# Performance work log

Measured on AMD Instinct MI355X. Metric: run time of the kernel, lower is better.

Reference implementation:

```python
import jax, jax.numpy as jnp
import numpy as np

B, T, D, H = 64, 512, 2048, 512

def setup_inputs() -> dict:
    key = jax.random.key(0)
    k1, k2, k3, k4, k5 = jax.random.split(key, 5)
    hidden_frames = jax.random.normal(k1, (B, T, D), dtype=jnp.float32)
    hidden_text = jax.random.normal(k2, (B, D), dtype=jnp.float32)
    Wa = jax.random.normal(k3, (D, H), dtype=jnp.float32) * 0.01
    Ua = jax.random.normal(k4, (D, H), dtype=jnp.float32) * 0.01
    Va = jax.random.normal(k5, (H,), dtype=jnp.float32) * 0.01
    ba = jnp.zeros((1, 1, H), dtype=jnp.float32)
    return {"hidden_frames": hidden_frames, "hidden_text": hidden_text,
            "Wa": Wa, "Ua": Ua, "Va": Va, "ba": ba}

def reference(hidden_frames, hidden_text, Wa, Ua, Va, ba):
    # Uh: [B, 1, H]
    Uh = jnp.matmul(hidden_text, Ua)[:, None, :]
    # Ws: [B, T, H]
    Ws = jnp.einsum('btd,dh->bth', hidden_frames, Wa)
    # additive attention scores: [B, T]
    scores = jnp.einsum('bth,h->bt', jnp.tanh(Ws + Uh + ba), Va)
    att = jax.nn.softmax(scores, axis=1)  # [B, T]
    # weighted sum over frames: [B, D]
    return jnp.einsum('bt,btd->bd', att, hidden_frames)
```

## Files before the change

### kernel.cpp

```cpp
#include <hip/hip_runtime.h>
#include <hip/hip_bf16.h>
#include <stdint.h>

#define B_ 64
#define T_ 512
#define D_ 2048
#define H_ 512

typedef __bf16 bf16x8 __attribute__((ext_vector_type(8)));
typedef float floatx4 __attribute__((ext_vector_type(4)));

__device__ __forceinline__ unsigned short f2bf(float f) {
  unsigned int u = __float_as_uint(f);
  return (unsigned short)((u + 0x7FFFu + ((u >> 16) & 1u)) >> 16);
}
__device__ __forceinline__ unsigned int pack2(float a, float b) {
  return (unsigned int)f2bf(a) | ((unsigned int)f2bf(b) << 16);
}

__global__ void k_transpose_wa(const float* __restrict__ Wa,
                               unsigned short* __restrict__ WaT) {
  __shared__ float t[32][33];
  int h0 = blockIdx.x * 32;
  int d0 = blockIdx.y * 32;
  int j  = threadIdx.x & 31;
  int i0 = threadIdx.x >> 5;
#pragma unroll
  for (int ii = 0; ii < 4; ii++) {
    int i = i0 + ii * 8;
    t[i][j] = Wa[(size_t)(d0 + i) * H_ + h0 + j];
  }
  __syncthreads();
#pragma unroll
  for (int jj = 0; jj < 4; jj++) {
    int r = i0 + jj * 8;
    WaT[(size_t)(h0 + r) * D_ + d0 + j] = f2bf(t[j][r]);
  }
}

__global__ void k_uh(const float* __restrict__ text, const float* __restrict__ Ua,
                     float* __restrict__ UhB) {
  __shared__ float tloc[8][128];
  const int h  = blockIdx.x * 256 + threadIdx.x;
  const int b0 = blockIdx.y * 8;
  const int d0 = blockIdx.z * 128;
  {
    int r = threadIdx.x >> 5;
    int c = threadIdx.x & 31;
#pragma unroll
    for (int j = 0; j < 4; j++)
      tloc[r][c + 32 * j] = text[(size_t)(b0 + r) * D_ + d0 + c + 32 * j];
  }
  __syncthreads();
  float acc[8] = {0.f, 0.f, 0.f, 0.f, 0.f, 0.f, 0.f, 0.f};
#pragma unroll 4
  for (int dd = 0; dd < 128; dd++) {
    float ua = Ua[(size_t)(d0 + dd) * H_ + h];
#pragma unroll
    for (int i = 0; i < 8; i++) acc[i] = fmaf(tloc[i][dd], ua, acc[i]);
  }
#pragma unroll
  for (int i = 0; i < 8; i++) atomicAdd(&UhB[(b0 + i) * H_ + h], acc[i]);
}

__launch_bounds__(256, 2)
__global__ void k_scores(const float* __restrict__ frames,
                         const unsigned short* __restrict__ WaT,
                         const float* __restrict__ UhB,
                         const float* __restrict__ Va,
                         const float* __restrict__ ba,
                         float* __restrict__ scores) {
  __shared__ __align__(16) unsigned short ldsA[128 * 72];
  __shared__ __align__(16) unsigned short ldsB[128 * 72];
  const int tid  = threadIdx.x;
  const int lane = tid & 63, wave = tid >> 6;
  const int wm = wave >> 1, wn = wave & 1;
  const int lr = lane & 15, q = lane >> 4;
  const int mBase = blockIdx.x * 128;
  const int hBase = blockIdx.y * 128;

  floatx4 acc[4][4];
#pragma unroll
  for (int mi = 0; mi < 4; mi++)
#pragma unroll
    for (int ni = 0; ni < 4; ni++) acc[mi][ni] = (floatx4){0.f, 0.f, 0.f, 0.f};

  for (int k0 = 0; k0 < D_; k0 += 64) {
#pragma unroll
    for (int i = 0; i < 4; i++) {
      int task = i * 256 + tid;
      int m = task >> 3, oct = task & 7;
      const float* src = frames + (size_t)(mBase + m) * D_ + k0 + oct * 8;
      float4 p0 = ((const float4*)src)[0];
      float4 p1 = ((const float4*)src)[1];
      uint4 w;
      w.x = pack2(p0.x, p0.y); w.y = pack2(p0.z, p0.w);
      w.z = pack2(p1.x, p1.y); w.w = pack2(p1.z, p1.w);
      *reinterpret_cast<uint4*>(&ldsA[m * 72 + oct * 8]) = w;
    }
#pragma unroll
    for (int i = 0; i < 4; i++) {
      int task = i * 256 + tid;
      int n = task >> 3, oct = task & 7;
      uint4 w = *reinterpret_cast<const uint4*>(
          WaT + (size_t)(hBase + n) * D_ + k0 + oct * 8);
      *reinterpret_cast<uint4*>(&ldsB[n * 72 + oct * 8]) = w;
    }
    __syncthreads();
#pragma unroll
    for (int kk = 0; kk < 2; kk++) {
      bf16x8 af[4], bfr[4];
#pragma unroll
      for (int mi = 0; mi < 4; mi++)
        af[mi] = *reinterpret_cast<const bf16x8*>(
            &ldsA[(wm * 64 + mi * 16 + lr) * 72 + kk * 32 + q * 8]);
#pragma unroll
      for (int ni = 0; ni < 4; ni++)
        bfr[ni] = *reinterpret_cast<const bf16x8*>(
            &ldsB[(wn * 64 + ni * 16 + lr) * 72 + kk * 32 + q * 8]);
#pragma unroll
      for (int mi = 0; mi < 4; mi++)
#pragma unroll
        for (int ni = 0; ni < 4; ni++)
          acc[mi][ni] = __builtin_amdgcn_mfma_f32_16x16x32_bf16(
              af[mi], bfr[ni], acc[mi][ni], 0, 0, 0);
    }
    __syncthreads();
  }

  const int b = mBase >> 9;
  float uhv[4], vav[4];
#pragma unroll
  for (int ni = 0; ni < 4; ni++) {
    int h = hBase + wn * 64 + ni * 16 + lr;
    uhv[ni] = UhB[b * H_ + h] + ba[h];
    vav[ni] = Va[h];
  }
  const int rowBase = mBase + wm * 64;
#pragma unroll
  for (int mi = 0; mi < 4; mi++) {
#pragma unroll
    for (int reg = 0; reg < 4; reg++) {
      float s = 0.f;
#pragma unroll
      for (int ni = 0; ni < 4; ni++) {
        float x = acc[mi][ni][reg] + uhv[ni];
        float e = __expf(2.f * x);
        s += (1.f - 2.f / (e + 1.f)) * vav[ni];
      }
      s += __shfl_xor(s, 1, 16);
      s += __shfl_xor(s, 2, 16);
      s += __shfl_xor(s, 4, 16);
      s += __shfl_xor(s, 8, 16);
      if (lr == 0)
        atomicAdd(&scores[rowBase + mi * 16 + q * 4 + reg], s);
    }
  }
}

__global__ void k_softmax(const float* __restrict__ scores, float* __restrict__ att) {
  __shared__ float red[4];
  int b = blockIdx.x, tid = threadIdx.x;
  int lane = tid & 63, wave = tid >> 6;
  float s0 = scores[b * T_ + tid];
  float s1 = scores[b * T_ + 256 + tid];
  float mx = fmaxf(s0, s1);
#pragma unroll
  for (int off = 32; off; off >>= 1) mx = fmaxf(mx, __shfl_xor(mx, off, 64));
  if (lane == 0) red[wave] = mx;
  __syncthreads();
  mx = fmaxf(fmaxf(red[0], red[1]), fmaxf(red[2], red[3]));
  __syncthreads();
  float e0 = __expf(s0 - mx), e1 = __expf(s1 - mx);
  float sm = e0 + e1;
#pragma unroll
  for (int off = 32; off; off >>= 1) sm += __shfl_xor(sm, off, 64);
  if (lane == 0) red[wave] = sm;
  __syncthreads();
  sm = red[0] + red[1] + red[2] + red[3];
  float inv = 1.f / sm;
  att[b * T_ + tid]       = e0 * inv;
  att[b * T_ + 256 + tid] = e1 * inv;
}

__global__ void k_wsum(const float* __restrict__ frames, const float* __restrict__ att,
                       float* __restrict__ out) {
  int b  = blockIdx.y;
  int d0 = blockIdx.x * 1024 + threadIdx.x * 4;
  int t0 = blockIdx.z * (T_ / 4);
  const float* fp = frames + (size_t)b * T_ * D_ + d0;
  const float* ap = att + b * T_;
  float4 acc = {0.f, 0.f, 0.f, 0.f};
  for (int t = t0; t < t0 + T_ / 4; t += 4) {
    float a0 = ap[t], a1 = ap[t + 1], a2 = ap[t + 2], a3 = ap[t + 3];
    float4 v0 = *(const float4*)(fp + (size_t)(t + 0) * D_);
    float4 v1 = *(const float4*)(fp + (size_t)(t + 1) * D_);
    float4 v2 = *(const float4*)(fp + (size_t)(t + 2) * D_);
    float4 v3 = *(const float4*)(fp + (size_t)(t + 3) * D_);
    acc.x += a0 * v0.x + a1 * v1.x + a2 * v2.x + a3 * v3.x;
    acc.y += a0 * v0.y + a1 * v1.y + a2 * v2.y + a3 * v3.y;
    acc.z += a0 * v0.z + a1 * v1.z + a2 * v2.z + a3 * v3.z;
    acc.w += a0 * v0.w + a1 * v1.w + a2 * v2.w + a3 * v3.w;
  }
  float* op = out + (size_t)b * D_ + d0;
  atomicAdd(op + 0, acc.x);
  atomicAdd(op + 1, acc.y);
  atomicAdd(op + 2, acc.z);
  atomicAdd(op + 3, acc.w);
}

extern "C" void kernel_launch(void* const* d_in, const int* in_sizes, int n_in,
                              void* d_out, int out_size, void* d_ws, size_t ws_size,
                              hipStream_t stream) {
  const float* frames = (const float*)d_in[0];
  const float* text   = (const float*)d_in[1];
  const float* Wa     = (const float*)d_in[2];
  const float* Ua     = (const float*)d_in[3];
  const float* Va     = (const float*)d_in[4];
  const float* ba     = (const float*)d_in[5];
  float* out = (float*)d_out;

  char* ws = (char*)d_ws;
  unsigned short* WaT = (unsigned short*)ws;
  float* UhB    = (float*)(ws + (size_t)(2u << 20));
  float* scores = (float*)(ws + (size_t)(2u << 20) + (128u << 10));
  float* att    = (float*)(ws + (size_t)(2u << 20) + (256u << 10));

  (void)hipMemsetAsync(UhB, 0, (size_t)(256u << 10), stream);
  (void)hipMemsetAsync(out, 0, (size_t)B_ * D_ * sizeof(float), stream);

  k_transpose_wa<<<dim3(H_ / 32, D_ / 32), 256, 0, stream>>>(Wa, WaT);
  k_uh<<<dim3(H_ / 256, B_ / 8, D_ / 128), 256, 0, stream>>>(text, Ua, UhB);
  k_scores<<<dim3((B_ * T_) / 128, H_ / 128), 256, 0, stream>>>(frames, WaT, UhB, Va, ba, scores);
  k_softmax<<<B_, 256, 0, stream>>>(scores, att);
  k_wsum<<<dim3(D_ / 1024, B_, 4), 256, 0, stream>>>(frames, att, out);
}
```

Before: 630.5 us.

## Precast frames to bf16 and load GEMM tiles with direct global-to-LDS loads

Adds a pass that casts the fp32 frames to bf16 in the workspace once, so the scores GEMM, which rereads frames for each of four H tiles, reads half the bytes and skips the per-tile conversion. Both A and B tiles are now loaded with global_load_lds 16-byte transfers straight into LDS, and the LDS row padding goes from 72 to 64 elements to match. This costs an extra 256MB write and reread of the cast buffer, and the unpadded LDS layout may cause bank conflicts on the fragment reads. The cast path only runs if the workspace is large enough, otherwise the old fp32 path is kept.

Measured after the change: 579.8 us. 1.09x faster.

```diff
diff --git a/kernel.cpp b/kernel.cpp
--- a/kernel.cpp
+++ b/kernel.cpp
@@ -16,6 +16,12 @@
 }
 __device__ __forceinline__ unsigned int pack2(float a, float b) {
   return (unsigned int)f2bf(a) | ((unsigned int)f2bf(b) << 16);
+}
+
+__device__ __forceinline__ void gload16(const void* g, void* l) {
+  __builtin_amdgcn_global_load_lds(
+      (const __attribute__((address_space(1))) void*)g,
+      (__attribute__((address_space(3))) void*)l, 16, 0, 0);
 }
 
 __global__ void k_transpose_wa(const float* __restrict__ Wa,
@@ -36,6 +42,16 @@
     int r = i0 + jj * 8;
     WaT[(size_t)(h0 + r) * D_ + d0 + j] = f2bf(t[j][r]);
   }
+}
+
+__global__ void k_cast(const float* __restrict__ in, unsigned short* __restrict__ out) {
+  size_t i = ((size_t)blockIdx.x * 256 + threadIdx.x) * 8;
+  float4 a = ((const float4*)(in + i))[0];
+  float4 b = ((const float4*)(in + i))[1];
+  uint4 w;
+  w.x = pack2(a.x, a.y); w.y = pack2(a.z, a.w);
+  w.z = pack2(b.x, b.y); w.w = pack2(b.z, b.w);
+  *(uint4*)(out + i) = w;
 }
 
 __global__ void k_uh(const float* __restrict__ text, const float* __restrict__ Ua,
@@ -63,15 +79,16 @@
   for (int i = 0; i < 8; i++) atomicAdd(&UhB[(b0 + i) * H_ + h], acc[i]);
 }
 
+template <bool PRECAST>
 __launch_bounds__(256, 2)
-__global__ void k_scores(const float* __restrict__ frames,
+__global__ void k_scores(const void* __restrict__ framesAny,
                          const unsigned short* __restrict__ WaT,
                          const float* __restrict__ UhB,
                          const float* __restrict__ Va,
                          const float* __restrict__ ba,
                          float* __restrict__ scores) {
-  __shared__ __align__(16) unsigned short ldsA[128 * 72];
-  __shared__ __align__(16) unsigned short ldsB[128 * 72];
+  __shared__ __align__(16) unsigned short ldsA[128 * 64];
+  __shared__ __align__(16) unsigned short ldsB[128 * 64];
   const int tid  = threadIdx.x;
   const int lane = tid & 63, wave = tid >> 6;
   const int wm = wave >> 1, wn = wave & 1;
@@ -79,6 +96,8 @@
   const int mBase = blockIdx.x * 128;
   const int hBase = blockIdx.y * 128;
 
+  const int sRow = lane >> 3, sOct = lane & 7;
+
   floatx4 acc[4][4];
 #pragma unroll
   for (int mi = 0; mi < 4; mi++)
@@ -86,25 +105,34 @@
     for (int ni = 0; ni < 4; ni++) acc[mi][ni] = (floatx4){0.f, 0.f, 0.f, 0.f};
 
   for (int k0 = 0; k0 < D_; k0 += 64) {
+    if (PRECAST) {
+      const unsigned short* fb = (const unsigned short*)framesAny;
+#pragma unroll
+      for (int i = 0; i < 4; i++) {
+        int r0 = wave * 32 + i * 8;
+        gload16(fb + (size_t)(mBase + r0 + sRow) * D_ + k0 + sOct * 8,
+                &ldsA[r0 * 64]);
+      }
+    } else {
+      const float* ff = (const float*)framesAny;
+#pragma unroll
+      for (int i = 0; i < 4; i++) {
+        int task = i * 256 + tid;
+        int m = task >> 3, oct = task & 7;
+        const float* src = ff + (size_t)(mBase + m) * D_ + k0 + oct * 8;
+        float4 p0 = ((const float4*)src)[0];
+        float4 p1 = ((const float4*)src)[1];
+        uint4 w;
+        w.x = pack2(p0.x, p0.y); w.y = pack2(p0.z, p0.w);
+        w.z = pack2(p1.x, p1.y); w.w = pack2(p1.z, p1.w);
+        *reinterpret_cast<uint4*>(&ldsA[m * 64 + oct * 8]) = w;
+      }
+    }
 #pragma unroll
     for (int i = 0; i < 4; i++) {
-      int task = i * 256 + tid;
-      int m = task >> 3, oct = task & 7;
-      const float* src = frames + (size_t)(mBase + m) * D_ + k0 + oct * 8;
-      float4 p0 = ((const float4*)src)[0];
-      float4 p1 = ((const float4*)src)[1];
-      uint4 w;
-      w.x = pack2(p0.x, p0.y); w.y = pack2(p0.z, p0.w);
-      w.z = pack2(p1.x, p1.y); w.w = pack2(p1.z, p1.w);
-      *reinterpret_cast<uint4*>(&ldsA[m * 72 + oct * 8]) = w;
-    }
-#pragma unroll
-    for (int i = 0; i < 4; i++) {
-      int task = i * 256 + tid;
-      int n = task >> 3, oct = task & 7;
-      uint4 w = *reinterpret_cast<const uint4*>(
-          WaT + (size_t)(hBase + n) * D_ + k0 + oct * 8);
-      *reinterpret_cast<uint4*>(&ldsB[n * 72 + oct * 8]) = w;
+      int r0 = wave * 32 + i * 8;
+      gload16(WaT + (size_t)(hBase + r0 + sRow) * D_ + k0 + sOct * 8,
+              &ldsB[r0 * 64]);
     }
     __syncthreads();
 #pragma unroll
@@ -113,11 +141,11 @@
 #pragma unroll
       for (int mi = 0; mi < 4; mi++)
         af[mi] = *reinterpret_cast<const bf16x8*>(
-            &ldsA[(wm * 64 + mi * 16 + lr) * 72 + kk * 32 + q * 8]);
+            &ldsA[(wm * 64 + mi * 16 + lr) * 64 + kk * 32 + q * 8]);
 #pragma unroll
       for (int ni = 0; ni < 4; ni++)
         bfr[ni] = *reinterpret_cast<const bf16x8*>(
-            &ldsB[(wn * 64 + ni * 16 + lr) * 72 + kk * 32 + q * 8]);
+            &ldsB[(wn * 64 + ni * 16 + lr) * 64 + kk * 32 + q * 8]);
 #pragma unroll
       for (int mi = 0; mi < 4; mi++)
 #pragma unroll
@@ -220,18 +248,30 @@
   const float* ba     = (const float*)d_in[5];
   float* out = (float*)d_out;
 
+  const size_t FRAMES_BF_BYTES = (size_t)B_ * T_ * D_ * 2;
+  const bool precast = ws_size >= FRAMES_BF_BYTES + (4u << 20);
+
   char* ws = (char*)d_ws;
-  unsigned short* WaT = (unsigned short*)ws;
-  float* UhB    = (float*)(ws + (size_t)(2u << 20));
-  float* scores = (float*)(ws + (size_t)(2u << 20) + (128u << 10));
-  float* att    = (float*)(ws + (size_t)(2u << 20) + (256u << 10));
+  unsigned short* framesBf = (unsigned short*)ws;
+  size_t off = precast ? FRAMES_BF_BYTES : 0;
+  unsigned short* WaT = (unsigned short*)(ws + off);          off += (2u << 20);
+  float* UhB    = (float*)(ws + off);                         off += (128u << 10);
+  float* scores = (float*)(ws + off);                         off += (128u << 10);
+  float* att    = (float*)(ws + off);
 
   (void)hipMemsetAsync(UhB, 0, (size_t)(256u << 10), stream);
   (void)hipMemsetAsync(out, 0, (size_t)B_ * D_ * sizeof(float), stream);
 
   k_transpose_wa<<<dim3(H_ / 32, D_ / 32), 256, 0, stream>>>(Wa, WaT);
   k_uh<<<dim3(H_ / 256, B_ / 8, D_ / 128), 256, 0, stream>>>(text, Ua, UhB);
-  k_scores<<<dim3((B_ * T_) / 128, H_ / 128), 256, 0, stream>>>(frames, WaT, UhB, Va, ba, scores);
+  if (precast) {
+    k_cast<<<(B_ * T_ * D_) / (256 * 8), 256, 0, stream>>>(frames, framesBf);
+    k_scores<true><<<dim3((B_ * T_) / 128, H_ / 128), 256, 0, stream>>>(
+        framesBf, WaT, UhB, Va, ba, scores);
+  } else {
+    k_scores<false><<<dim3((B_ * T_) / 128, H_ / 128), 256, 0, stream>>>(
+        frames, WaT, UhB, Va, ba, scores);
+  }
   k_softmax<<<B_, 256, 0, stream>>>(scores, att);
   k_wsum<<<dim3(D_ / 1024, B_, 4), 256, 0, stream>>>(frames, att, out);
 }
```
